# Performance work log

Measured on AMD Instinct MI355X. Metric: run time of the kernel, lower is better.

Reference implementation:

```python
import jax, jax.numpy as jnp
import numpy as np

B, T, H = 16, 512, 2048


def setup_inputs() -> dict:
    key = jax.random.key(0)
    kx, kw, kb = jax.random.split(key, 3)
    x = jax.random.normal(kx, (B, T, H), dtype=jnp.float32)
    # scale like nn.Linear default init so the linear recurrence is stable over T steps
    W = jax.random.normal(kw, (H, 2 * H), dtype=jnp.float32) / jnp.sqrt(2.0 * H)
    b = jax.random.normal(kb, (H,), dtype=jnp.float32) * 0.01
    return {"x": x, "W": W, "b": b}


def reference(x, W, b):
    # torch: h_t = Linear([x_t ; h_{t-1}]) = [x_t ; h_{t-1}] @ W.T + b
    # split W (H, 2H) into Wx (H, H) acting on x and Wh (H, H) acting on h
    Hh = x.shape[-1]
    Wx, Wh = W[:, :Hh], W[:, Hh:]
    # hoist the input projection out of the recurrence: one big GEMM
    u = jnp.einsum('bth,gh->btg', x, Wx) + b  # (B, T, H)
    h0 = jnp.zeros((x.shape[0], Hh), dtype=x.dtype)

    def step(h, u_t):
        h = u_t + h @ Wh.T  # affine recurrence, no nonlinearity (matches source)
        return h, h

    h_last, outs = jax.lax.scan(step, h0, jnp.swapaxes(u, 0, 1))  # outs: (T, B, H)
    out = jnp.swapaxes(outs, 0, 1)  # (B, T, H), batch_first
    return out, h_last
```

## Files before the change

### kernel.cpp

```cpp
#include <hip/hip_runtime.h>
#include <hip/hip_fp16.h>
#include <stdint.h>

#define HDIM 2048
#define BATCH 16
#define TLEN 512
#define TH   1048576
#define OUT_MAIN 16777216

using floatx4 = __attribute__((ext_vector_type(4))) float;
using shortx8 = __attribute__((ext_vector_type(8))) short;
using halfx8  = __attribute__((ext_vector_type(8))) _Float16;
typedef unsigned long long ull;

static __device__ __forceinline__ unsigned f16bits(float f) {
    _Float16 h = (_Float16)f;
    return (unsigned)*(unsigned short*)&h;
}

__global__ void cast_x_kernel(const float* __restrict__ x, _Float16* __restrict__ xh, int n) {
    int i = blockIdx.x * blockDim.x + threadIdx.x;
    int stride = gridDim.x * blockDim.x;
    for (; i < n; i += stride) xh[i] = (_Float16)x[i];
}

__global__ void cast_w_kernel(const float* __restrict__ W,
                              _Float16* __restrict__ wxh,
                              _Float16* __restrict__ whh) {
    int i = blockIdx.x * blockDim.x + threadIdx.x;
    int stride = gridDim.x * blockDim.x;
    for (; i < HDIM * HDIM; i += stride) {
        int g = i >> 11, k = i & (HDIM - 1);
        wxh[i] = (_Float16)W[g * (2 * HDIM) + k];
        whh[i] = (_Float16)W[g * (2 * HDIM) + HDIM + k];
    }
}

__global__ void transpose_wh_kernel(const float* __restrict__ W,
                                    _Float16* __restrict__ whT) {
    __shared__ float tile[32][33];
    int bx = blockIdx.x * 32, by = blockIdx.y * 32;
    int tx = threadIdx.x, ty = threadIdx.y;
#pragma unroll
    for (int r = 0; r < 32; r += 8)
        tile[ty + r][tx] = W[(size_t)(by + ty + r) * (2 * HDIM) + HDIM + bx + tx];
    __syncthreads();
#pragma unroll
    for (int r = 0; r < 32; r += 8)
        whT[(size_t)(bx + ty + r) * HDIM + by + tx] = (_Float16)tile[tx][ty + r];
}

__global__ __launch_bounds__(256) void gemm_u_kernel(
    const _Float16* __restrict__ xh,
    const _Float16* __restrict__ wxh,
    const float* __restrict__ bias,
    float* __restrict__ out,
    _Float16* __restrict__ uh)
{
    __shared__ __align__(16) short As[4 * 128 * 8];
    __shared__ __align__(16) short Bs[4 * 128 * 8];

    const int j = threadIdx.x;
    const int m0 = blockIdx.x * 128;
    const int n0 = blockIdx.y * 128;
    const int w = j >> 6, lane = j & 63;
    const int wm = (w >> 1) * 64, wn = (w & 1) * 64;
    const int quad = lane >> 4, l15 = lane & 15;

    const int mA0 = j & 127, kg0 = j >> 7;
    const int mA1 = (j + 256) & 127, kg1 = (j + 256) >> 7;

    floatx4 acc[4][4] = {};

    shortx8 ra0 = *(const shortx8*)(xh  + (size_t)(m0 + mA0) * HDIM + kg0 * 8);
    shortx8 ra1 = *(const shortx8*)(xh  + (size_t)(m0 + mA1) * HDIM + kg1 * 8);
    shortx8 rb0 = *(const shortx8*)(wxh + (size_t)(n0 + mA0) * HDIM + kg0 * 8);
    shortx8 rb1 = *(const shortx8*)(wxh + (size_t)(n0 + mA1) * HDIM + kg1 * 8);

    for (int kt = 0; kt < 64; ++kt) {
        ((shortx8*)As)[kg0 * 128 + mA0] = ra0;
        ((shortx8*)As)[kg1 * 128 + mA1] = ra1;
        ((shortx8*)Bs)[kg0 * 128 + mA0] = rb0;
        ((shortx8*)Bs)[kg1 * 128 + mA1] = rb1;
        __syncthreads();

        if (kt < 63) {
            int k = (kt + 1) * 32;
            ra0 = *(const shortx8*)(xh  + (size_t)(m0 + mA0) * HDIM + k + kg0 * 8);
            ra1 = *(const shortx8*)(xh  + (size_t)(m0 + mA1) * HDIM + k + kg1 * 8);
            rb0 = *(const shortx8*)(wxh + (size_t)(n0 + mA0) * HDIM + k + kg0 * 8);
            rb1 = *(const shortx8*)(wxh + (size_t)(n0 + mA1) * HDIM + k + kg1 * 8);
        }

        halfx8 af[4], bf[4];
#pragma unroll
        for (int mt = 0; mt < 4; ++mt)
            af[mt] = ((const halfx8*)As)[quad * 128 + wm + mt * 16 + l15];
#pragma unroll
        for (int nt = 0; nt < 4; ++nt)
            bf[nt] = ((const halfx8*)Bs)[quad * 128 + wn + nt * 16 + l15];
#pragma unroll
        for (int mt = 0; mt < 4; ++mt)
#pragma unroll
            for (int nt = 0; nt < 4; ++nt)
                acc[mt][nt] = __builtin_amdgcn_mfma_f32_16x16x32_f16(af[mt], bf[nt], acc[mt][nt], 0, 0, 0);
        __syncthreads();
    }

#pragma unroll
    for (int nt = 0; nt < 4; ++nt) {
        int gn = n0 + wn + nt * 16 + l15;
        float bv = bias[gn];
#pragma unroll
        for (int mt = 0; mt < 4; ++mt) {
#pragma unroll
            for (int r = 0; r < 4; ++r) {
                int gm = m0 + wm + mt * 16 + quad * 4 + r;
                float v = acc[mt][nt][r] + bv;
                out[(size_t)gm * HDIM + gn] = v;
                uh[(size_t)gm * HDIM + gn] = (_Float16)v;
            }
        }
    }
}

__global__ __launch_bounds__(256) void gemm_w2_kernel(
    const _Float16* __restrict__ whh,
    const _Float16* __restrict__ wT,
    _Float16* __restrict__ w2)
{
    __shared__ __align__(16) short As[4 * 128 * 8];
    __shared__ __align__(16) short Bs[4 * 128 * 8];

    const int j = threadIdx.x;
    const int m0 = blockIdx.x * 128;
    const int n0 = blockIdx.y * 128;
    const int w = j >> 6, lane = j & 63;
    const int wm = (w >> 1) * 64, wn = (w & 1) * 64;
    const int quad = lane >> 4, l15 = lane & 15;

    const int mA0 = j & 127, kg0 = j >> 7;
    const int mA1 = (j + 256) & 127, kg1 = (j + 256) >> 7;

    floatx4 acc[4][4] = {};

    shortx8 ra0 = *(const shortx8*)(whh + (size_t)(m0 + mA0) * HDIM + kg0 * 8);
    shortx8 ra1 = *(const shortx8*)(whh + (size_t)(m0 + mA1) * HDIM + kg1 * 8);
    shortx8 rb0 = *(const shortx8*)(wT  + (size_t)(n0 + mA0) * HDIM + kg0 * 8);
    shortx8 rb1 = *(const shortx8*)(wT  + (size_t)(n0 + mA1) * HDIM + kg1 * 8);

    for (int kt = 0; kt < 64; ++kt) {
        ((shortx8*)As)[kg0 * 128 + mA0] = ra0;
        ((shortx8*)As)[kg1 * 128 + mA1] = ra1;
        ((shortx8*)Bs)[kg0 * 128 + mA0] = rb0;
        ((shortx8*)Bs)[kg1 * 128 + mA1] = rb1;
        __syncthreads();

        if (kt < 63) {
            int k = (kt + 1) * 32;
            ra0 = *(const shortx8*)(whh + (size_t)(m0 + mA0) * HDIM + k + kg0 * 8);
            ra1 = *(const shortx8*)(whh + (size_t)(m0 + mA1) * HDIM + k + kg1 * 8);
            rb0 = *(const shortx8*)(wT  + (size_t)(n0 + mA0) * HDIM + k + kg0 * 8);
            rb1 = *(const shortx8*)(wT  + (size_t)(n0 + mA1) * HDIM + k + kg1 * 8);
        }

        halfx8 af[4], bf[4];
#pragma unroll
        for (int mt = 0; mt < 4; ++mt)
            af[mt] = ((const halfx8*)As)[quad * 128 + wm + mt * 16 + l15];
#pragma unroll
        for (int nt = 0; nt < 4; ++nt)
            bf[nt] = ((const halfx8*)Bs)[quad * 128 + wn + nt * 16 + l15];
#pragma unroll
        for (int mt = 0; mt < 4; ++mt)
#pragma unroll
            for (int nt = 0; nt < 4; ++nt)
                acc[mt][nt] = __builtin_amdgcn_mfma_f32_16x16x32_f16(af[mt], bf[nt], acc[mt][nt], 0, 0, 0);
        __syncthreads();
    }

#pragma unroll
    for (int nt = 0; nt < 4; ++nt) {
        int gn = n0 + wn + nt * 16 + l15;
#pragma unroll
        for (int mt = 0; mt < 4; ++mt)
#pragma unroll
            for (int r = 0; r < 4; ++r) {
                int gm = m0 + wm + mt * 16 + quad * 4 + r;
                w2[(size_t)gm * HDIM + gn] = (_Float16)acc[mt][nt][r];
            }
    }
}

__global__ __launch_bounds__(256) void gemm_v_kernel(
    const _Float16* __restrict__ uh,
    const _Float16* __restrict__ whh,
    float* __restrict__ out)
{
    __shared__ __align__(16) short As[4 * 128 * 8];
    __shared__ __align__(16) short Bs[4 * 128 * 8];

    const int j = threadIdx.x;
    const int m0 = blockIdx.x * 128;
    const int n0 = blockIdx.y * 128;
    const int w = j >> 6, lane = j & 63;
    const int wm = (w >> 1) * 64, wn = (w & 1) * 64;
    const int quad = lane >> 4, l15 = lane & 15;

    const int mA0 = j & 127, kg0 = j >> 7;
    const int mA1 = (j + 256) & 127, kg1 = (j + 256) >> 7;

    int rowA0 = m0 + mA0 - 1; if (rowA0 < 0) rowA0 = 0;
    int rowA1 = m0 + mA1 - 1; if (rowA1 < 0) rowA1 = 0;

    floatx4 acc[4][4] = {};

    shortx8 ra0 = *(const shortx8*)(uh  + (size_t)rowA0 * HDIM + kg0 * 8);
    shortx8 ra1 = *(const shortx8*)(uh  + (size_t)rowA1 * HDIM + kg1 * 8);
    shortx8 rb0 = *(const shortx8*)(whh + (size_t)(n0 + mA0) * HDIM + kg0 * 8);
    shortx8 rb1 = *(const shortx8*)(whh + (size_t)(n0 + mA1) * HDIM + kg1 * 8);

    for (int kt = 0; kt < 64; ++kt) {
        ((shortx8*)As)[kg0 * 128 + mA0] = ra0;
        ((shortx8*)As)[kg1 * 128 + mA1] = ra1;
        ((shortx8*)Bs)[kg0 * 128 + mA0] = rb0;
        ((shortx8*)Bs)[kg1 * 128 + mA1] = rb1;
        __syncthreads();

        if (kt < 63) {
            int k = (kt + 1) * 32;
            ra0 = *(const shortx8*)(uh  + (size_t)rowA0 * HDIM + k + kg0 * 8);
            ra1 = *(const shortx8*)(uh  + (size_t)rowA1 * HDIM + k + kg1 * 8);
            rb0 = *(const shortx8*)(whh + (size_t)(n0 + mA0) * HDIM + k + kg0 * 8);
            rb1 = *(const shortx8*)(whh + (size_t)(n0 + mA1) * HDIM + k + kg1 * 8);
        }

        halfx8 af[4], bf[4];
#pragma unroll
        for (int mt = 0; mt < 4; ++mt)
            af[mt] = ((const halfx8*)As)[quad * 128 + wm + mt * 16 + l15];
#pragma unroll
        for (int nt = 0; nt < 4; ++nt)
            bf[nt] = ((const halfx8*)Bs)[quad * 128 + wn + nt * 16 + l15];
#pragma unroll
        for (int mt = 0; mt < 4; ++mt)
#pragma unroll
            for (int nt = 0; nt < 4; ++nt)
                acc[mt][nt] = __builtin_amdgcn_mfma_f32_16x16x32_f16(af[mt], bf[nt], acc[mt][nt], 0, 0, 0);
        __syncthreads();
    }

#pragma unroll
    for (int nt = 0; nt < 4; ++nt) {
        int gn = n0 + wn + nt * 16 + l15;
#pragma unroll
        for (int mt = 0; mt < 4; ++mt)
#pragma unroll
            for (int r = 0; r < 4; ++r) {
                int gm = m0 + wm + mt * 16 + quad * 4 + r;
                float uval = out[(size_t)gm * HDIM + gn];
                float res = ((gm & 511) == 0) ? uval : (acc[mt][nt][r] + uval);
                out[(size_t)gm * HDIM + gn] = res;
            }
    }
}

__global__ __launch_bounds__(1024) void rnn_scan_kernel(
    const _Float16* __restrict__ w2,
    short* __restrict__ ring,
    float* __restrict__ out,
    unsigned* __restrict__ flags)
{
    __shared__ float ps[16 * 4 * 16 * 17];

    const int j = threadIdx.x;
    const int w = j >> 6, lane = j & 63;
    const int quad = lane >> 4, l15 = lane & 15;
    const int chain = blockIdx.x & 1;
    const int rank = blockIdx.x >> 1;
    const int n0 = rank * 64;

    unsigned* myflag = flags + (chain * 32 + rank) * 32;
    const unsigned* pollbase = flags + chain * 32 * 32;

    halfx8 af[4][4];
#pragma unroll
    for (int gt = 0; gt < 4; ++gt)
#pragma unroll
        for (int c = 0; c < 4; ++c) {
            int row = n0 + gt * 16 + l15;
            int k = w * 128 + c * 32 + quad * 8;
            af[gt][c] = *(const halfx8*)(w2 + (size_t)row * HDIM + k);
        }

    const int rn = j & 63, rb = j >> 6;
    const int gt_r = rn >> 4, row_r = rn & 15;

    for (int s = 0; s < 256; ++s) {
        const int t = chain + 2 * s;
        short* slot_next = ring + (size_t)(s * 2 + chain) * 32768;

        float uv = out[(size_t)rb * TH + (size_t)t * HDIM + n0 + rn];

        floatx4 acc[4][2] = {};
        if (s > 0) {
            const short* slot_prev = ring + (size_t)((s - 1) * 2 + chain) * 32768;
            if (lane < 2) {
                const unsigned* fp = pollbase + (w * 2 + lane) * 32;
                while (__hip_atomic_load(fp, __ATOMIC_RELAXED, __HIP_MEMORY_SCOPE_AGENT) < (unsigned)s) {}
            }
            __asm__ __volatile__("" ::: "memory");

#pragma unroll
            for (int c = 0; c < 4; ++c) {
                int kg = w * 16 + c * 4 + quad;
                halfx8 bh = *(const halfx8*)(slot_prev + kg * 128 + l15 * 8);
                int cp = c & 1;
                acc[0][cp] = __builtin_amdgcn_mfma_f32_16x16x32_f16(af[0][c], bh, acc[0][cp], 0, 0, 0);
                acc[1][cp] = __builtin_amdgcn_mfma_f32_16x16x32_f16(af[1][c], bh, acc[1][cp], 0, 0, 0);
                acc[2][cp] = __builtin_amdgcn_mfma_f32_16x16x32_f16(af[2][c], bh, acc[2][cp], 0, 0, 0);
                acc[3][cp] = __builtin_amdgcn_mfma_f32_16x16x32_f16(af[3][c], bh, acc[3][cp], 0, 0, 0);
            }
        }

#pragma unroll
        for (int gt = 0; gt < 4; ++gt) {
            floatx4 a = acc[gt][0] + acc[gt][1];
#pragma unroll
            for (int r = 0; r < 4; ++r)
                ps[((w * 4 + gt) * 16 + quad * 4 + r) * 17 + l15] = a[r];
        }
        __syncthreads();

        float sv_f = uv;
#pragma unroll
        for (int ww = 0; ww < 16; ++ww)
            sv_f += ps[((ww * 4 + gt_r) * 16 + row_r) * 17 + rb];

        int n = n0 + rn;

        unsigned hb = f16bits(sv_f);
        unsigned hb2 = __shfl_down(hb, 1);
        if ((j & 1) == 0) {
            int idx = (n >> 3) * 128 + rb * 8 + (n & 7);
            __hip_atomic_store((unsigned*)(slot_next + idx), hb | (hb2 << 16),
                               __ATOMIC_RELAXED, __HIP_MEMORY_SCOPE_AGENT);
        }

        __syncthreads();
        if (j == 0)
            __hip_atomic_store(myflag, (unsigned)(s + 1), __ATOMIC_RELAXED, __HIP_MEMORY_SCOPE_AGENT);

        out[(size_t)rb * TH + (size_t)t * HDIM + n] = sv_f;
        if (t == TLEN - 1) out[(size_t)OUT_MAIN + (size_t)rb * HDIM + n] = sv_f;
    }
}

extern "C" void kernel_launch(void* const* d_in, const int* in_sizes, int n_in,
                              void* d_out, int out_size, void* d_ws, size_t ws_size,
                              hipStream_t stream) {
    (void)in_sizes; (void)n_in; (void)out_size; (void)ws_size;
    const float* x    = (const float*)d_in[0];
    const float* W    = (const float*)d_in[1];
    const float* bias = (const float*)d_in[2];
    float* out = (float*)d_out;
    char* ws = (char*)d_ws;

    _Float16* xh  = (_Float16*)(ws);
    _Float16* whT = (_Float16*)(ws);
    _Float16* w2  = (_Float16*)(ws + 8388608);
    short*    ring = (short*)(ws + 16777216);
    _Float16* wxh = (_Float16*)(ws + 33554432);
    _Float16* whh = (_Float16*)(ws + 41943040);
    _Float16* uh  = (_Float16*)(ws + 50331648);
    unsigned* flags = (unsigned*)(ws + 83886080);

    hipMemsetAsync(ws + 83886080, 0, 16384, stream);

    cast_x_kernel<<<8192, 256, 0, stream>>>(x, xh, OUT_MAIN);
    cast_w_kernel<<<8192, 256, 0, stream>>>(W, wxh, whh);
    gemm_u_kernel<<<dim3(64, 16), 256, 0, stream>>>(xh, wxh, bias, out, uh);
    transpose_wh_kernel<<<dim3(64, 64), dim3(32, 8), 0, stream>>>(W, whT);
    gemm_v_kernel<<<dim3(64, 16), 256, 0, stream>>>(uh, whh, out);
    gemm_w2_kernel<<<dim3(16, 16), 256, 0, stream>>>(whh, whT, w2);
    rnn_scan_kernel<<<64, 1024, 0, stream>>>(w2, ring, out, flags);
}
```

Measured before the change: 1.148 ms.

## Split scan into batch groups with 128 blocks of 512 threads and row-major ring

The recurrent scan now runs 128 blocks of 512 threads instead of 64 blocks of 1024. Each block handles 8 of the 16 batch rows for a 64-column slice, and each wave covers a 256-wide k range, holding twice the weight fragments in registers. The ring buffer switches to a plain batch-major layout written with 64-bit packed stores, and each block polls only the flags of its own batch group. The aim is to spread the serial recurrence over more CUs with shorter cross-wave reductions, at the cost of half-used MFMA B operands (only 8 of 16 columns are valid), higher register pressure and more blocks in the flag synchronisation.

```diff
diff --git a/kernel.cpp b/kernel.cpp
--- a/kernel.cpp
+++ b/kernel.cpp
@@ -265,56 +265,59 @@
     }
 }
 
-__global__ __launch_bounds__(1024) void rnn_scan_kernel(
+__global__ __launch_bounds__(512, 2) void rnn_scan_kernel(
     const _Float16* __restrict__ w2,
     short* __restrict__ ring,
     float* __restrict__ out,
     unsigned* __restrict__ flags)
 {
-    __shared__ float ps[16 * 4 * 16 * 17];
+    __shared__ float ps[8 * 4 * 16 * 9];
 
     const int j = threadIdx.x;
     const int w = j >> 6, lane = j & 63;
     const int quad = lane >> 4, l15 = lane & 15;
     const int chain = blockIdx.x & 1;
     const int rank = blockIdx.x >> 1;
-    const int n0 = rank * 64;
-
-    unsigned* myflag = flags + (chain * 32 + rank) * 32;
-    const unsigned* pollbase = flags + chain * 32 * 32;
-
-    halfx8 af[4][4];
+    const int bg = rank >> 5;
+    const int cg = rank & 31;
+    const int n0 = cg * 64;
+    const int b0 = bg * 8;
+
+    unsigned* myflag = flags + (chain * 64 + rank) * 32;
+    const unsigned* pollbase = flags + chain * 64 * 32;
+
+    halfx8 af[4][8];
 #pragma unroll
     for (int gt = 0; gt < 4; ++gt)
 #pragma unroll
-        for (int c = 0; c < 4; ++c) {
+        for (int c = 0; c < 8; ++c) {
             int row = n0 + gt * 16 + l15;
-            int k = w * 128 + c * 32 + quad * 8;
+            int k = w * 256 + c * 32 + quad * 8;
             af[gt][c] = *(const halfx8*)(w2 + (size_t)row * HDIM + k);
         }
 
-    const int rn = j & 63, rb = j >> 6;
-    const int gt_r = rn >> 4, row_r = rn & 15;
+    const int col_r = j & 63, b_r = j >> 6;
+    const int gt_r = col_r >> 4, row_r = col_r & 15;
+    const int mybatch = b0 + (l15 & 7);
 
     for (int s = 0; s < 256; ++s) {
         const int t = chain + 2 * s;
         short* slot_next = ring + (size_t)(s * 2 + chain) * 32768;
 
-        float uv = out[(size_t)rb * TH + (size_t)t * HDIM + n0 + rn];
+        float uv = out[(size_t)(b0 + b_r) * TH + (size_t)t * HDIM + n0 + col_r];
 
         floatx4 acc[4][2] = {};
         if (s > 0) {
             const short* slot_prev = ring + (size_t)((s - 1) * 2 + chain) * 32768;
-            if (lane < 2) {
-                const unsigned* fp = pollbase + (w * 2 + lane) * 32;
+            if (lane < 4) {
+                const unsigned* fp = pollbase + (bg * 32 + w * 4 + lane) * 32;
                 while (__hip_atomic_load(fp, __ATOMIC_RELAXED, __HIP_MEMORY_SCOPE_AGENT) < (unsigned)s) {}
             }
             __asm__ __volatile__("" ::: "memory");
 
 #pragma unroll
-            for (int c = 0; c < 4; ++c) {
-                int kg = w * 16 + c * 4 + quad;
-                halfx8 bh = *(const halfx8*)(slot_prev + kg * 128 + l15 * 8);
+            for (int c = 0; c < 8; ++c) {
+                halfx8 bh = *(const halfx8*)(slot_prev + mybatch * 2048 + w * 256 + c * 32 + quad * 8);
                 int cp = c & 1;
                 acc[0][cp] = __builtin_amdgcn_mfma_f32_16x16x32_f16(af[0][c], bh, acc[0][cp], 0, 0, 0);
                 acc[1][cp] = __builtin_amdgcn_mfma_f32_16x16x32_f16(af[1][c], bh, acc[1][cp], 0, 0, 0);
@@ -326,24 +329,27 @@
 #pragma unroll
         for (int gt = 0; gt < 4; ++gt) {
             floatx4 a = acc[gt][0] + acc[gt][1];
-#pragma unroll
-            for (int r = 0; r < 4; ++r)
-                ps[((w * 4 + gt) * 16 + quad * 4 + r) * 17 + l15] = a[r];
+            if (l15 < 8) {
+#pragma unroll
+                for (int r = 0; r < 4; ++r)
+                    ps[((w * 4 + gt) * 16 + quad * 4 + r) * 9 + l15] = a[r];
+            }
         }
         __syncthreads();
 
         float sv_f = uv;
 #pragma unroll
-        for (int ww = 0; ww < 16; ++ww)
-            sv_f += ps[((ww * 4 + gt_r) * 16 + row_r) * 17 + rb];
-
-        int n = n0 + rn;
+        for (int ww = 0; ww < 8; ++ww)
+            sv_f += ps[((ww * 4 + gt_r) * 16 + row_r) * 9 + b_r];
 
         unsigned hb = f16bits(sv_f);
-        unsigned hb2 = __shfl_down(hb, 1);
-        if ((j & 1) == 0) {
-            int idx = (n >> 3) * 128 + rb * 8 + (n & 7);
-            __hip_atomic_store((unsigned*)(slot_next + idx), hb | (hb2 << 16),
+        unsigned h1 = __shfl_down(hb, 1);
+        unsigned h2 = __shfl_down(hb, 2);
+        unsigned h3 = __shfl_down(hb, 3);
+        if ((j & 3) == 0) {
+            size_t idx = (size_t)(b0 + b_r) * 2048 + n0 + col_r;
+            ull pk = (ull)(hb | (h1 << 16)) | (((ull)(h2 | (h3 << 16))) << 32);
+            __hip_atomic_store((ull*)(slot_next + idx), pk,
                                __ATOMIC_RELAXED, __HIP_MEMORY_SCOPE_AGENT);
         }
 
@@ -351,8 +357,8 @@
         if (j == 0)
             __hip_atomic_store(myflag, (unsigned)(s + 1), __ATOMIC_RELAXED, __HIP_MEMORY_SCOPE_AGENT);
 
-        out[(size_t)rb * TH + (size_t)t * HDIM + n] = sv_f;
-        if (t == TLEN - 1) out[(size_t)OUT_MAIN + (size_t)rb * HDIM + n] = sv_f;
+        out[(size_t)(b0 + b_r) * TH + (size_t)t * HDIM + n0 + col_r] = sv_f;
+        if (t == TLEN - 1) out[(size_t)OUT_MAIN + (size_t)(b0 + b_r) * HDIM + n0 + col_r] = sv_f;
     }
 }
 
@@ -383,5 +389,5 @@
     transpose_wh_kernel<<<dim3(64, 64), dim3(32, 8), 0, stream>>>(W, whT);
     gemm_v_kernel<<<dim3(64, 16), 256, 0, stream>>>(uh, whh, out);
     gemm_w2_kernel<<<dim3(16, 16), 256, 0, stream>>>(whh, whT, w2);
-    rnn_scan_kernel<<<64, 1024, 0, stream>>>(w2, ring, out, flags);
-}
+    rnn_scan_kernel<<<128, 512, 0, stream>>>(w2, ring, out, flags);
+}
```

Result: slower. 1.310 ms (+14.1%).
